# Kernel tuning notes

Hardware: AMD Instinct MI355X
Metric: run time of the kernel (lower is better)

The kernel has to match this reference:

```python
import jax, jax.numpy as jnp
import numpy as np

USER = 100000
ITEM = 100000
LATDIM = 64
ETYPE = 8
GNN_LAYERS = 2
HYPER_NUM = 128
N_EDGES = 100000


def setup_inputs() -> dict:
    key = jax.random.key(0)
    ks = jax.random.split(key, 7)
    # xavier-ish scaled params
    uEmbeds = jax.random.normal(ks[0], (USER, LATDIM), dtype=jnp.float32) * 0.05
    iEmbeds = jax.random.normal(ks[1], (ITEM, LATDIM), dtype=jnp.float32) * 0.05
    edgeTrans = jax.random.normal(ks[2], (ETYPE, LATDIM, LATDIM), dtype=jnp.float32) * 0.1
    src = jax.random.randint(ks[3], (N_EDGES,), 0, USER, dtype=jnp.int64 if jax.config.jax_enable_x64 else jnp.int32)
    tgt = jax.random.randint(ks[4], (N_EDGES,), 0, ITEM, dtype=src.dtype)
    val = jax.random.randint(ks[5], (N_EDGES,), 0, ETYPE, dtype=src.dtype)
    hyper = jax.random.normal(ks[6], (N_EDGES, HYPER_NUM), dtype=jnp.float32)
    return {"uEmbeds": uEmbeds, "iEmbeds": iEmbeds, "edgeTrans": edgeTrans,
            "hyper": hyper, "src": src, "tgt": tgt, "val": val}


def _hgnn_layer(edgeEmbeds, hyper):
    act = lambda x: jax.nn.leaky_relu(x, 0.5)
    # [d, H] = embeds^T @ hyper
    hyperEmbeds = act(jnp.einsum('ed,eh->dh', edgeEmbeds, hyper))
    # [E, d] = (hyperEmbeds @ hyper^T)^T
    nodeEmbeds = act(jnp.einsum('eh,dh->ed', hyper, hyperEmbeds))
    return nodeEmbeds


def reference(uEmbeds, iEmbeds, edgeTrans, hyper, src, tgt, val):
    srcE = uEmbeds[src]                       # [E, d] gather
    trans = edgeTrans[val]                    # [E, d, d] gather (large)
    # per-edge row-vector x matrix, then elementwise mult with tgt embeds
    edgeEmbeds = jnp.einsum('ed,edk->ek', srcE, trans) * iEmbeds[tgt]  # [E, d]
    for _ in range(GNN_LAYERS):
        edgeEmbeds = _hgnn_layer(edgeEmbeds, hyper) + edgeEmbeds
    srcOut = jax.ops.segment_sum(edgeEmbeds, src, num_segments=USER)  # sparse.sum over dim 1
    tgtOut = jax.ops.segment_sum(edgeEmbeds, tgt, num_segments=ITEM)  # sparse.sum over dim 0
    return (srcOut, tgtOut)
```

## Files before the change

### kernel.cpp

```cpp
#include <hip/hip_runtime.h>

#define E_N     100000
#define USER_N  100000
#define NROW    200000
#define NB_ACC  256
#define BIN_CAP 16384
#define E_PAD   114688
#define ACC_NCH 7
#define ACC_CHUNK 64
#define BUCKET_CAP 16
#define NB_INIT 782
#define NB_CONV 1792

typedef __bf16 bf16x8 __attribute__((ext_vector_type(8)));
typedef __bf16 bf16x4 __attribute__((ext_vector_type(4)));
typedef float  f32x4  __attribute__((ext_vector_type(4)));

__device__ __forceinline__ float leaky(float x) { return x > 0.f ? x : 0.5f * x; }

__global__ void __launch_bounds__(256) prepKernel(
    int* __restrict__ cnt, int* __restrict__ cnt8,
    const float* __restrict__ T, __bf16* __restrict__ Tt,
    const float* __restrict__ hyper, __bf16* __restrict__ hyperT,
    __bf16* __restrict__ hyperB) {
  __shared__ __bf16 sT[128][72];
  const int b = blockIdx.x;
  const int tid = threadIdx.x;
  if (b < NB_INIT) {
    const int i = b * 256 + tid;
    if (i < NROW + 2) cnt[i] = 0;
    if (i < 8) cnt8[i] = 0;
    if (b < 8) {
      const float* Tv = T + (size_t)b * 4096;
      __bf16* Tb = Tt + (size_t)b * 4096;
      for (int idx = tid; idx < 4096; idx += 256) {
        const int d = idx >> 6, k = idx & 63;
        Tb[k * 64 + d] = (__bf16)Tv[idx];
      }
    }
    return;
  }
  const int cb = b - NB_INIT;
  const int e0 = cb * 64;
  const int h = tid >> 1, eoff = (tid & 1) * 32;
  if (e0 >= E_N) {
    const float4 z = make_float4(0.f, 0.f, 0.f, 0.f);
    #pragma unroll
    for (int q = 0; q < 4; ++q)
      *(float4*)((char*)(hyperT + (size_t)h * E_PAD + e0 + eoff) + q * 16) = z;
    return;
  }
  float4 v[8];
  #pragma unroll
  for (int r = 0; r < 8; ++r) {
    const int idx = r * 256 + tid;
    const int e = idx >> 5, h4 = (idx & 31) * 4;
    v[r] = make_float4(0.f, 0.f, 0.f, 0.f);
    if (e0 + e < E_N) v[r] = *(const float4*)(hyper + (size_t)(e0 + e) * 128 + h4);
  }
  #pragma unroll
  for (int r = 0; r < 8; ++r) {
    const int idx = r * 256 + tid;
    const int e = idx >> 5, h4 = (idx & 31) * 4;
    const int ce = e ^ ((idx & 15) * 4);
    bf16x4 pk;
    pk[0] = (__bf16)v[r].x; pk[1] = (__bf16)v[r].y;
    pk[2] = (__bf16)v[r].z; pk[3] = (__bf16)v[r].w;
    if (e0 + e < E_N)
      *(bf16x4*)(hyperB + (size_t)(e0 + e) * 128 + h4) = pk;
    sT[h4 + 0][ce] = pk[0]; sT[h4 + 1][ce] = pk[1];
    sT[h4 + 2][ce] = pk[2]; sT[h4 + 3][ce] = pk[3];
  }
  __syncthreads();
  const int swz = ((h >> 2) & 15) * 4;
  #pragma unroll
  for (int q = 0; q < 8; ++q) {
    const bf16x4 vv = *(const bf16x4*)&sT[h][(eoff + q * 4) ^ swz];
    *(bf16x4*)(hyperT + (size_t)h * E_PAD + e0 + eoff + q * 4) = vv;
  }
}

__global__ void binKernel(const int* __restrict__ val, const int* __restrict__ src,
                          const int* __restrict__ tgt,
                          int* __restrict__ perm, int* __restrict__ permSrc,
                          int* __restrict__ permTgt,
                          int* __restrict__ cnt8, int* __restrict__ cnt,
                          int* __restrict__ list) {
  __shared__ int lh[8], lbase[8];
  const int tid = threadIdx.x;
  if (tid < 8) lh[tid] = 0;
  __syncthreads();
  const int e = blockIdx.x * 256 + tid;
  int v = -1, slot = 0, s = 0, t = 0;
  if (e < E_N) {
    v = val[e]; s = src[e]; t = tgt[e];
    slot = atomicAdd(&lh[v], 1);
    const int ps = atomicAdd(&cnt[s], 1);
    if (ps < BUCKET_CAP) list[(size_t)s * BUCKET_CAP + ps] = e;
    const int pt = atomicAdd(&cnt[USER_N + t], 1);
    if (pt < BUCKET_CAP) list[(size_t)(USER_N + t) * BUCKET_CAP + pt] = e;
  }
  __syncthreads();
  if (tid < 8) lbase[tid] = atomicAdd(&cnt8[tid], lh[tid]);
  __syncthreads();
  if (v >= 0) {
    const int p = v * BIN_CAP + lbase[v] + slot;
    perm[p] = e; permSrc[p] = s; permTgt[p] = t;
  }
}

__global__ void __launch_bounds__(256) stageAMfmaKernel(
    const float* __restrict__ uE, const float* __restrict__ iE, const __bf16* __restrict__ Tt,
    const int* __restrict__ permSrc, const int* __restrict__ permTgt,
    const int* __restrict__ perm, const int* __restrict__ cnt8,
    float* __restrict__ edge) {
  __shared__ float sC[4][16][68];
  const int v  = blockIdx.y;
  const int nE = min(cnt8[v], BIN_CAP);
  const int tid  = threadIdx.x;
  const int lane = tid & 63;
  const int wave = tid >> 6;
  const int l16 = lane & 15, quad = lane >> 4;
  const int wbase = blockIdx.x * 128 + wave * 32;
  if (wbase >= nE) return;

  bf16x8 Bf[2][4];
  #pragma unroll
  for (int kc = 0; kc < 2; ++kc)
    #pragma unroll
    for (int nt = 0; nt < 4; ++nt)
      Bf[kc][nt] = *(const bf16x8*)(Tt + (size_t)v * 4096 + (nt * 16 + l16) * 64 + kc * 32 + quad * 8);

  int sI[2], tI[2], eI[2];
  #pragma unroll
  for (int s = 0; s < 2; ++s) {
    const int eoffS = wbase + s * 16;
    const bool lv = (eoffS + l16 < nE);
    const int p = v * BIN_CAP + (lv ? eoffS + l16 : 0);
    sI[s] = permSrc[p]; tI[s] = permTgt[p]; eI[s] = perm[p];
  }

  float4 f0[2][2], f1[2][2];
  #pragma unroll
  for (int s = 0; s < 2; ++s)
    #pragma unroll
    for (int kc = 0; kc < 2; ++kc) {
      const float* ap = uE + (size_t)sI[s] * 64 + kc * 32 + quad * 8;
      f0[s][kc] = *(const float4*)ap;
      f1[s][kc] = *(const float4*)(ap + 4);
    }

  const int r  = lane >> 2;
  const int c0 = (lane & 3) * 4;

  float4 iv[2][4];
  int tj2[2], gj2[2];
  #pragma unroll
  for (int sh = 0; sh < 2; ++sh) {
    tj2[sh] = __shfl(tI[sh], r, 64);
    gj2[sh] = __shfl(eI[sh], r, 64);
    #pragma unroll
    for (int q = 0; q < 4; ++q)
      iv[sh][q] = *(const float4*)(iE + (size_t)tj2[sh] * 64 + c0 + q * 16);
  }

  f32x4 acc[2][4];
  #pragma unroll
  for (int sh = 0; sh < 2; ++sh)
    #pragma unroll
    for (int nt = 0; nt < 4; ++nt) acc[sh][nt] = (f32x4){0.f, 0.f, 0.f, 0.f};
  #pragma unroll
  for (int sh = 0; sh < 2; ++sh) {
    #pragma unroll
    for (int kc = 0; kc < 2; ++kc) {
      bf16x8 a;
      a[0] = (__bf16)f0[sh][kc].x; a[1] = (__bf16)f0[sh][kc].y;
      a[2] = (__bf16)f0[sh][kc].z; a[3] = (__bf16)f0[sh][kc].w;
      a[4] = (__bf16)f1[sh][kc].x; a[5] = (__bf16)f1[sh][kc].y;
      a[6] = (__bf16)f1[sh][kc].z; a[7] = (__bf16)f1[sh][kc].w;
      #pragma unroll
      for (int nt = 0; nt < 4; ++nt)
        acc[sh][nt] = __builtin_amdgcn_mfma_f32_16x16x32_bf16(a, Bf[kc][nt], acc[sh][nt], 0, 0, 0);
    }
  }
  #pragma unroll
  for (int sh = 0; sh < 2; ++sh) {
    const int eoffS = wbase + sh * 16;
    #pragma unroll
    for (int nt = 0; nt < 4; ++nt)
      #pragma unroll
      for (int reg = 0; reg < 4; ++reg)
        sC[wave][quad * 4 + reg][nt * 16 + l16] = acc[sh][nt][reg];
    if (eoffS + r < nE) {
      #pragma unroll
      for (int q = 0; q < 4; ++q) {
        const int c = c0 + q * 16;
        const float4 cv = *(const float4*)&sC[wave][r][c];
        float4 rr;
        rr.x = cv.x * iv[sh][q].x; rr.y = cv.y * iv[sh][q].y;
        rr.z = cv.z * iv[sh][q].z; rr.w = cv.w * iv[sh][q].w;
        *(float4*)(edge + (size_t)gj2[sh] * 64 + c) = rr;
      }
    }
  }
}

__global__ void __launch_bounds__(512) hyperAccumMfmaKernel(
    const float* __restrict__ edge, const __bf16* __restrict__ hyperT,
    float* __restrict__ partials) {
  __shared__ __bf16 sE[2][64][72];
  const int tid  = threadIdx.x;
  const int lane = tid & 63;
  const int wave = tid >> 6;
  const int l16 = lane & 15, quad = lane >> 4;
  const int e0base = blockIdx.x * (ACC_NCH * ACC_CHUNK);
  const int d  = tid & 63;
  const int eg = tid >> 6;

  float rv[8];
  auto gload = [&](int c) {
    const int ebase = e0base + c * ACC_CHUNK + eg * 8;
    const float* p = edge + (size_t)ebase * 64 + d;
    if (ebase + 8 <= E_N) {
      #pragma unroll
      for (int i = 0; i < 8; ++i) rv[i] = p[i * 64];
    } else {
      #pragma unroll
      for (int i = 0; i < 8; ++i) rv[i] = (ebase + i < E_N) ? p[i * 64] : 0.f;
    }
  };
  auto swrite = [&](int b) {
    bf16x8 pk;
    #pragma unroll
    for (int i = 0; i < 8; ++i) pk[i] = (__bf16)rv[i];
    *(bf16x8*)&sE[b][d][eg * 8] = pk;
  };

  f32x4 acc[4];
  #pragma unroll
  for (int dt = 0; dt < 4; ++dt) acc[dt] = (f32x4){0.f, 0.f, 0.f, 0.f};

  gload(0); swrite(0);
  __syncthreads();
  for (int c = 0; c < ACC_NCH; ++c) {
    const int nb = c & 1;
    if (c + 1 < ACC_NCH) gload(c + 1);
    #pragma unroll
    for (int ks = 0; ks < 2; ++ks) {
      const int eoff = c * ACC_CHUNK + ks * 32 + quad * 8;
      const bf16x8 B = *(const bf16x8*)(hyperT + (size_t)(wave * 16 + l16) * E_PAD + e0base + eoff);
      bf16x8 A[4];
      #pragma unroll
      for (int dt = 0; dt < 4; ++dt)
        A[dt] = *(const bf16x8*)&sE[nb][dt * 16 + l16][ks * 32 + quad * 8];
      #pragma unroll
      for (int dt = 0; dt < 4; ++dt)
        acc[dt] = __builtin_amdgcn_mfma_f32_16x16x32_bf16(A[dt], B, acc[dt], 0, 0, 0);
    }
    if (c + 1 < ACC_NCH) {
      __syncthreads();
      swrite(nb ^ 1);
      __syncthreads();
    }
  }
  float* pp = partials + (size_t)blockIdx.x * 8192;
  const int h = wave * 16 + l16;
  #pragma unroll
  for (int dt = 0; dt < 4; ++dt)
    #pragma unroll
    for (int reg = 0; reg < 4; ++reg) {
      const int dd = dt * 16 + quad * 4 + reg;
      pp[dd * 128 + h] = acc[dt][reg];
    }
}

__global__ void __launch_bounds__(256) reduceKernel(const float* __restrict__ partials,
                                                    __bf16* __restrict__ HEtT) {
  __shared__ float sd[8][33];
  const int tid = threadIdx.x;
  const int o = blockIdx.x * 32 + (tid & 31);
  const int g = tid >> 5;
  float s = 0.f;
  #pragma unroll 4
  for (int b = g * 32; b < (g + 1) * 32; ++b) s += partials[(size_t)b * 8192 + o];
  sd[g][tid & 31] = s;
  __syncthreads();
  if (tid < 32) {
    float t = 0.f;
    #pragma unroll
    for (int k = 0; k < 8; ++k) t += sd[k][tid];
    HEtT[blockIdx.x * 32 + tid] = (__bf16)leaky(t);
  }
}

__global__ void __launch_bounds__(256) nodeUpdateMfmaKernel(
    const __bf16* __restrict__ HEtT, const __bf16* __restrict__ hyperB,
    float* __restrict__ edge) {
  const int tid  = threadIdx.x;
  const int lane = tid & 63;
  const int wave = tid >> 6;
  const int l16 = lane & 15, quad = lane >> 4;
  bf16x8 Bf[4][4];
  #pragma unroll
  for (int kc = 0; kc < 4; ++kc)
    #pragma unroll
    for (int dt = 0; dt < 4; ++dt)
      Bf[kc][dt] = *(const bf16x8*)(HEtT + (dt * 16 + l16) * 128 + kc * 32 + quad * 8);
  const int wv = blockIdx.x * 4 + wave;
  for (int t = wv; t < E_N / 16; t += 2048) {
    const int e0 = t * 16;
    bf16x8 A[4];
    #pragma unroll
    for (int kc = 0; kc < 4; ++kc)
      A[kc] = *(const bf16x8*)(hyperB + (size_t)(e0 + l16) * 128 + kc * 32 + quad * 8);
    f32x4 acc[4];
    #pragma unroll
    for (int dt = 0; dt < 4; ++dt) acc[dt] = (f32x4){0.f, 0.f, 0.f, 0.f};
    #pragma unroll
    for (int kc = 0; kc < 4; ++kc)
      #pragma unroll
      for (int dt = 0; dt < 4; ++dt)
        acc[dt] = __builtin_amdgcn_mfma_f32_16x16x32_bf16(A[kc], Bf[kc][dt], acc[dt], 0, 0, 0);
    #pragma unroll
    for (int dt = 0; dt < 4; ++dt) {
      const int d = dt * 16 + l16;
      #pragma unroll
      for (int reg = 0; reg < 4; ++reg) {
        const int e = e0 + quad * 4 + reg;
        float* ep = edge + (size_t)e * 64 + d;
        *ep = *ep + leaky(acc[dt][reg]);
      }
    }
  }
}

__global__ void gatherSumKernel(const float* __restrict__ edge,
                                const int* __restrict__ cnt,
                                const int* __restrict__ list,
                                float* __restrict__ out) {
  const int tid = threadIdx.x;
  const int sub = tid & 15;
  const int grpInWave = (tid >> 4) & 3;
  const int gid = blockIdx.x * 16 + (tid >> 4);
  const int nG = gridDim.x * 16;
  for (int r = gid; r < NROW; r += nG) {
    const int n = min(cnt[r], BUCKET_CAP);
    int eL = (sub < n) ? list[(size_t)r * BUCKET_CAP + sub] : 0;
    float4 acc = make_float4(0.f, 0.f, 0.f, 0.f);
    for (int i = 0; i < n; ++i) {
      const int e = __shfl(eL, grpInWave * 16 + i, 64);
      const float4 v = *(const float4*)(edge + (size_t)e * 64 + sub * 4);
      acc.x += v.x; acc.y += v.y; acc.z += v.z; acc.w += v.w;
    }
    *(float4*)(out + (size_t)r * 64 + sub * 4) = acc;
  }
}

extern "C" void kernel_launch(void* const* d_in, const int* in_sizes, int n_in,
                              void* d_out, int out_size, void* d_ws, size_t ws_size,
                              hipStream_t stream) {
  const float* uE    = (const float*)d_in[0];
  const float* iE    = (const float*)d_in[1];
  const float* T     = (const float*)d_in[2];
  const float* hyper = (const float*)d_in[3];
  const int*   src   = (const int*)d_in[4];
  const int*   tgt   = (const int*)d_in[5];
  const int*   val   = (const int*)d_in[6];
  float* out = (float*)d_out;
  float* ws  = (float*)d_ws;

  float*  edge     = ws;
  float*  partials = ws + 6400000;
  __bf16* HEtT     = (__bf16*)(ws + 6400000 + 4194304 + 65536);
  int* perm    = (int*)partials;
  int* permSrc = perm + 8 * BIN_CAP;
  int* permTgt = permSrc + 8 * BIN_CAP;
  int* cnt8    = permTgt + 8 * BIN_CAP;
  int* cnt  = (int*)(ws + 6400000 + 4194304 + 65536 + 4096);
  int* list = cnt + (NROW + 4);
  __bf16* hyperT = (__bf16*)(ws + 15136256);
  __bf16* hyperB = (__bf16*)(ws + 22476288);
  __bf16* Tt     = (__bf16*)(ws + 28876288);

  prepKernel<<<NB_INIT + NB_CONV, 256, 0, stream>>>(cnt, cnt8, T, Tt, hyper, hyperT, hyperB);
  binKernel<<<(E_N + 255) / 256, 256, 0, stream>>>(val, src, tgt, perm, permSrc, permTgt, cnt8, cnt, list);
  stageAMfmaKernel<<<dim3(BIN_CAP / 128, 8), 256, 0, stream>>>(uE, iE, Tt, permSrc, permTgt, perm, cnt8, edge);

  for (int layer = 0; layer < 2; ++layer) {
    hyperAccumMfmaKernel<<<NB_ACC, 512, 0, stream>>>(edge, hyperT, partials);
    reduceKernel<<<256, 256, 0, stream>>>(partials, HEtT);
    nodeUpdateMfmaKernel<<<512, 256, 0, stream>>>(HEtT, hyperB, edge);
  }

  gatherSumKernel<<<12500, 256, 0, stream>>>(edge, cnt, list, out);
}
```

Measured before the change: 283.2 us.

## Drop transposed hyper copy; transpose hyper tiles in shared memory inside accumulate kernel

The prep kernel no longer builds a transposed bf16 copy of the hyper matrix. It now only converts hyper to row-major bf16 with a simple grid-stride loop. The accumulate kernel loads row-major hyper tiles alongside the edge tiles and transposes them through a swizzled shared-memory buffer before the MFMA. This removes one full-size transposed write in prep but adds LDS transpose work and extra shared memory in each of the two accumulate passes.

```diff
diff --git a/kernel.cpp b/kernel.cpp
--- a/kernel.cpp
+++ b/kernel.cpp
@@ -5,7 +5,6 @@
 #define NROW    200000
 #define NB_ACC  256
 #define BIN_CAP 16384
-#define E_PAD   114688
 #define ACC_NCH 7
 #define ACC_CHUNK 64
 #define BUCKET_CAP 16
@@ -21,9 +20,7 @@
 __global__ void __launch_bounds__(256) prepKernel(
     int* __restrict__ cnt, int* __restrict__ cnt8,
     const float* __restrict__ T, __bf16* __restrict__ Tt,
-    const float* __restrict__ hyper, __bf16* __restrict__ hyperT,
-    __bf16* __restrict__ hyperB) {
-  __shared__ __bf16 sT[128][72];
+    const float* __restrict__ hyper, __bf16* __restrict__ hyperB) {
   const int b = blockIdx.x;
   const int tid = threadIdx.x;
   if (b < NB_INIT) {
@@ -40,43 +37,15 @@
     }
     return;
   }
-  const int cb = b - NB_INIT;
-  const int e0 = cb * 64;
-  const int h = tid >> 1, eoff = (tid & 1) * 32;
-  if (e0 >= E_N) {
-    const float4 z = make_float4(0.f, 0.f, 0.f, 0.f);
-    #pragma unroll
-    for (int q = 0; q < 4; ++q)
-      *(float4*)((char*)(hyperT + (size_t)h * E_PAD + e0 + eoff) + q * 16) = z;
-    return;
-  }
-  float4 v[8];
-  #pragma unroll
-  for (int r = 0; r < 8; ++r) {
-    const int idx = r * 256 + tid;
-    const int e = idx >> 5, h4 = (idx & 31) * 4;
-    v[r] = make_float4(0.f, 0.f, 0.f, 0.f);
-    if (e0 + e < E_N) v[r] = *(const float4*)(hyper + (size_t)(e0 + e) * 128 + h4);
-  }
-  #pragma unroll
-  for (int r = 0; r < 8; ++r) {
-    const int idx = r * 256 + tid;
-    const int e = idx >> 5, h4 = (idx & 31) * 4;
-    const int ce = e ^ ((idx & 15) * 4);
+  const int gtid = (b - NB_INIT) * 256 + tid;
+  const int stride = NB_CONV * 256;
+  const float4* h4 = (const float4*)hyper;
+  for (int i = gtid; i < E_N * 32; i += stride) {
+    const float4 v = h4[i];
     bf16x4 pk;
-    pk[0] = (__bf16)v[r].x; pk[1] = (__bf16)v[r].y;
-    pk[2] = (__bf16)v[r].z; pk[3] = (__bf16)v[r].w;
-    if (e0 + e < E_N)
-      *(bf16x4*)(hyperB + (size_t)(e0 + e) * 128 + h4) = pk;
-    sT[h4 + 0][ce] = pk[0]; sT[h4 + 1][ce] = pk[1];
-    sT[h4 + 2][ce] = pk[2]; sT[h4 + 3][ce] = pk[3];
-  }
-  __syncthreads();
-  const int swz = ((h >> 2) & 15) * 4;
-  #pragma unroll
-  for (int q = 0; q < 8; ++q) {
-    const bf16x4 vv = *(const bf16x4*)&sT[h][(eoff + q * 4) ^ swz];
-    *(bf16x4*)(hyperT + (size_t)h * E_PAD + e0 + eoff + q * 4) = vv;
+    pk[0] = (__bf16)v.x; pk[1] = (__bf16)v.y;
+    pk[2] = (__bf16)v.z; pk[3] = (__bf16)v.w;
+    *(bf16x4*)(hyperB + (size_t)i * 4) = pk;
   }
 }
 
@@ -206,9 +175,10 @@
 }
 
 __global__ void __launch_bounds__(512) hyperAccumMfmaKernel(
-    const float* __restrict__ edge, const __bf16* __restrict__ hyperT,
+    const float* __restrict__ edge, const __bf16* __restrict__ hyperB,
     float* __restrict__ partials) {
   __shared__ __bf16 sE[2][64][72];
+  __shared__ __bf16 sH[128][72];
   const int tid  = threadIdx.x;
   const int lane = tid & 63;
   const int wave = tid >> 6;
@@ -216,6 +186,9 @@
   const int e0base = blockIdx.x * (ACC_NCH * ACC_CHUNK);
   const int d  = tid & 63;
   const int eg = tid >> 6;
+  const int eh = tid >> 4;
+  const int h8 = (tid & 15) * 8;
+  const int hswz = 8 * ((tid & 15) & 7);
 
   float rv[8];
   auto gload = [&](int c) {
@@ -236,19 +209,46 @@
     *(bf16x8*)&sE[b][d][eg * 8] = pk;
   };
 
+  bf16x8 hv[2];
+  auto hload = [&](int c) {
+    #pragma unroll
+    for (int p = 0; p < 2; ++p) {
+      const int e = e0base + c * ACC_CHUNK + p * 32 + eh;
+      if (e < E_N) {
+        hv[p] = *(const bf16x8*)(hyperB + (size_t)e * 128 + h8);
+      } else {
+        bf16x8 z;
+        #pragma unroll
+        for (int i = 0; i < 8; ++i) z[i] = (__bf16)0.f;
+        hv[p] = z;
+      }
+    }
+  };
+  auto hwrite = [&]() {
+    #pragma unroll
+    for (int p = 0; p < 2; ++p) {
+      const int ee = (p * 32 + eh) ^ hswz;
+      #pragma unroll
+      for (int j = 0; j < 8; ++j) sH[h8 + j][ee] = hv[p][j];
+    }
+  };
+
   f32x4 acc[4];
   #pragma unroll
   for (int dt = 0; dt < 4; ++dt) acc[dt] = (f32x4){0.f, 0.f, 0.f, 0.f};
 
-  gload(0); swrite(0);
+  const int hh = wave * 16 + l16;
+  const int bswz = 8 * ((hh >> 3) & 7);
+
+  gload(0); hload(0);
+  swrite(0); hwrite();
   __syncthreads();
   for (int c = 0; c < ACC_NCH; ++c) {
     const int nb = c & 1;
-    if (c + 1 < ACC_NCH) gload(c + 1);
+    if (c + 1 < ACC_NCH) { gload(c + 1); hload(c + 1); }
     #pragma unroll
     for (int ks = 0; ks < 2; ++ks) {
-      const int eoff = c * ACC_CHUNK + ks * 32 + quad * 8;
-      const bf16x8 B = *(const bf16x8*)(hyperT + (size_t)(wave * 16 + l16) * E_PAD + e0base + eoff);
+      const bf16x8 B = *(const bf16x8*)&sH[hh][(ks * 32 + quad * 8) ^ bswz];
       bf16x8 A[4];
       #pragma unroll
       for (int dt = 0; dt < 4; ++dt)
@@ -259,7 +259,7 @@
     }
     if (c + 1 < ACC_NCH) {
       __syncthreads();
-      swrite(nb ^ 1);
+      swrite(nb ^ 1); hwrite();
       __syncthreads();
     }
   }
@@ -378,16 +378,15 @@
   int* cnt8    = permTgt + 8 * BIN_CAP;
   int* cnt  = (int*)(ws + 6400000 + 4194304 + 65536 + 4096);
   int* list = cnt + (NROW + 4);
-  __bf16* hyperT = (__bf16*)(ws + 15136256);
   __bf16* hyperB = (__bf16*)(ws + 22476288);
   __bf16* Tt     = (__bf16*)(ws + 28876288);
 
-  prepKernel<<<NB_INIT + NB_CONV, 256, 0, stream>>>(cnt, cnt8, T, Tt, hyper, hyperT, hyperB);
+  prepKernel<<<NB_INIT + NB_CONV, 256, 0, stream>>>(cnt, cnt8, T, Tt, hyper, hyperB);
   binKernel<<<(E_N + 255) / 256, 256, 0, stream>>>(val, src, tgt, perm, permSrc, permTgt, cnt8, cnt, list);
   stageAMfmaKernel<<<dim3(BIN_CAP / 128, 8), 256, 0, stream>>>(uE, iE, Tt, permSrc, permTgt, perm, cnt8, edge);
 
   for (int layer = 0; layer < 2; ++layer) {
-    hyperAccumMfmaKernel<<<NB_ACC, 512, 0, stream>>>(edge, hyperT, partials);
+    hyperAccumMfmaKernel<<<NB_ACC, 512, 0, stream>>>(edge, hyperB, partials);
     reduceKernel<<<256, 256, 0, stream>>>(partials, HEtT);
     nodeUpdateMfmaKernel<<<512, 256, 0, stream>>>(HEtT, hyperB, edge);
   }
```

After: 275.3 us. -2.8%, faster.
